# Performance work log

Hardware: AMD Instinct MI355X
Metric: run time of the kernel (lower is better)

Reference implementation:

```python
import jax, jax.numpy as jnp
import numpy as np

NEG = jnp.finfo(jnp.float32).min


def setup_inputs() -> dict:
    key = jax.random.key(0)
    k1, k2, k3 = jax.random.split(key, 3)
    B, H, S, D = 1, 12, 4096, 64
    query = jax.random.normal(k1, (B, H, S, D), dtype=jnp.float32)
    key_t = jax.random.normal(k2, (B, H, S, D), dtype=jnp.float32)
    value = jax.random.normal(k3, (B, H, S, D), dtype=jnp.float32)
    attention_mask = jnp.ones((B, S), dtype=jnp.int32)  # 2D mask -> causal branch
    return {
        "query": query,
        "key": key_t,
        "value": value,
        "attention_mask": attention_mask,
        "sliding_window": 128,
    }


def reference(query, key, value, attention_mask, sliding_window):
    # query/key/value: [B, H, S, D]
    B, H, S, D = query.shape
    scaling = 1.0 / jnp.sqrt(jnp.float32(D))
    # QK^T scaled: [B, H, S, S]
    attn_weights = jnp.einsum("bhqd,bhkd->bhqk", query, key) * scaling
    i = jnp.arange(S)[:, None]
    j = jnp.arange(S)[None, :]
    # 2D attention_mask branch: causal triu mask (values of mask not used)
    causal_mask = jnp.where(j > i, NEG, 0.0).astype(attn_weights.dtype)
    attn_weights = attn_weights + causal_mask
    # sliding window: row i allows columns [max(0, i - sw + 1), i]
    sw_allowed = (j >= i - sliding_window + 1) & (j <= i)
    sw_mask = jnp.where(sw_allowed, 0.0, NEG).astype(jnp.float32)
    attn_weights = attn_weights + sw_mask[None, None, :, :]
    # softmax in float32, cast back to query dtype
    attn_weights = jax.nn.softmax(attn_weights.astype(jnp.float32), axis=-1).astype(query.dtype)
    # probs @ V, then transpose heads: [B, S, H, D]
    attn_output = jnp.einsum("bhqk,bhkd->bhqd", attn_weights, value)
    attn_output = jnp.transpose(attn_output, (0, 2, 1, 3))
    return attn_output, attn_weights
```

## Files before the change

### kernel.cpp

```cpp
#include <hip/hip_runtime.h>
#include <math.h>

#define NH 12
#define SEQ 4096
#define DIM 64
#define SW 128
#define RPB 16
#define TPB 256
#define MAXK (RPB + SW - 1)
#define PSTRIDE 144
#define BAND_BLOCKS (NH * (SEQ / RPB))
#define FILL_BLOCKS 8448
#define PERIOD 15
#define NCHUNK ((size_t)NH * SEQ * (SEQ / 4))

typedef float v4f __attribute__((ext_vector_type(4)));

__global__ __launch_bounds__(TPB, 3)
void attn_fused3(const float* __restrict__ Q, const float* __restrict__ K,
                 const float* __restrict__ V, float* __restrict__ Wout,
                 float* __restrict__ Oout) {
    __shared__ v4f K4[MAXK * 16];
    __shared__ __align__(16) float Qs[RPB * DIM];
    __shared__ v4f Ps4[RPB * (PSTRIDE / 4)];
    float* Ps = (float*)Ps4;

    const int grp = blockIdx.x / PERIOD;
    const int rem = blockIdx.x % PERIOD;

    if (rem >= 4) {
        const size_t fid    = (size_t)grp * 11 + (rem - 4);
        const size_t tid0   = fid * TPB + threadIdx.x;
        const size_t stride = (size_t)FILL_BLOCKS * TPB;
        const float4 z = make_float4(0.f, 0.f, 0.f, 0.f);
        for (size_t idx = tid0; idx < NCHUNK; idx += stride) {
            const int ci = (int)(idx & 1023);
            const int i  = (int)((idx >> 10) & 4095);
            const int w0 = max(0, i - (SW - 1));
            if (ci < (w0 >> 2) || ci > (i >> 2)) {
                *(float4*)((float*)Wout + idx * 4) = z;
            }
        }
        return;
    }

    const int bid  = grp * 4 + rem;
    const int h    = bid / (SEQ / RPB);
    const int tile = bid % (SEQ / RPB);
    const int r0   = tile * RPB;
    const int kLo  = max(0, r0 - (SW - 1));
    const int nK   = r0 + RPB - kLo;

    const float* Qh = Q + (size_t)h * SEQ * DIM;
    const float* Kh = K + (size_t)h * SEQ * DIM;
    const float* Vh = V + (size_t)h * SEQ * DIM;
    const int tid = threadIdx.x;

    for (int idx = tid; idx < MAXK * 16; idx += TPB) {
        const int c = idx >> 4, b = idx & 15;
        const int src = min(c, nK - 1);
        K4[c * 16 + (b ^ (c & 15))] =
            *(const v4f*)(Kh + (size_t)(kLo + src) * DIM + b * 4);
    }
    {
        const int r = tid >> 4, b = tid & 15;
        *(v4f*)&Qs[r * 64 + b * 4] = *(const v4f*)(Qh + (size_t)(r0 + r) * DIM + b * 4);
    }
    __syncthreads();

    const int wave = tid >> 6;
    const int lane = tid & 63;
    const float scale = 0.125f;
    const int rbase = wave * 4;

    {
        const int base = rbase * (PSTRIDE / 4);
        for (int idx = lane; idx < 4 * (PSTRIDE / 4); idx += 64)
            Ps4[base + idx] = (v4f){0.f, 0.f, 0.f, 0.f};
    }

    for (int t = 0; t < 4; ++t) {
        const int r  = rbase + t;
        const int i  = r0 + r;
        const int w0 = max(0, i - (SW - 1));
        const int c0 = w0 - kLo;

        v4f q[16];
        #pragma unroll
        for (int b = 0; b < 16; ++b) q[b] = *(const v4f*)&Qs[r * 64 + b * 4];

        const int cA = c0 + lane;
        float accA = 0.f;
        #pragma unroll
        for (int b = 0; b < 16; ++b) {
            const v4f kv = K4[cA * 16 + (b ^ (cA & 15))];
            accA += q[b].x * kv.x + q[b].y * kv.y + q[b].z * kv.z + q[b].w * kv.w;
        }
        const int colA = w0 + lane;
        const float s0 = (colA <= i) ? accA * scale : -INFINITY;

        const int cB = cA + 64;
        float accB = 0.f;
        #pragma unroll
        for (int b = 0; b < 16; ++b) {
            const v4f kv = K4[cB * 16 + (b ^ (cB & 15))];
            accB += q[b].x * kv.x + q[b].y * kv.y + q[b].z * kv.z + q[b].w * kv.w;
        }
        const int colB = colA + 64;
        const float s1 = (colB <= i) ? accB * scale : -INFINITY;

        float m = fmaxf(s0, s1);
        #pragma unroll
        for (int o = 32; o > 0; o >>= 1) m = fmaxf(m, __shfl_xor(m, o, 64));
        const float e0 = __expf(s0 - m);
        const float e1 = __expf(s1 - m);
        float sum = e0 + e1;
        #pragma unroll
        for (int o = 32; o > 0; o >>= 1) sum += __shfl_xor(sum, o, 64);
        const float inv = 1.0f / sum;
        const float p0 = e0 * inv, p1 = e1 * inv;

        Ps[r * PSTRIDE + c0 + lane]      = p0;
        Ps[r * PSTRIDE + c0 + 64 + lane] = p1;

        float* wrow = Wout + ((size_t)h * SEQ + i) * SEQ;
        if (colA <= i) wrow[colA] = p0;
        if (colB <= i) wrow[colB] = p1;
        if (lane < 4) {
            const int cl = (w0 & ~3) + lane;
            if (cl < w0) wrow[cl] = 0.f;
            const int ch = i + 1 + lane;
            if (ch <= (i | 3)) wrow[ch] = 0.f;
        }
    }

    {
        const int i0  = r0 + rbase;
        const int u0k = max(0, i0 - (SW - 1)) - kLo;
        const int u1k = i0 + 3 - kLo;
        const int nch = (u1k - u0k + 4) >> 2;
        const int q4  = lane >> 4, l16 = lane & 15;

        v4f a0 = {0.f,0.f,0.f,0.f}, a1 = a0, a2 = a0, a3 = a0;
        for (int k = 0; k < nch; ++k) {
            const int cc   = u0k + k * 4 + q4;
            const int vrow = min(kLo + cc, SEQ - 1);
            const v4f vv = *(const v4f*)(Vh + (size_t)vrow * DIM + l16 * 4);
            a0 += Ps[(rbase + 0) * PSTRIDE + cc] * vv;
            a1 += Ps[(rbase + 1) * PSTRIDE + cc] * vv;
            a2 += Ps[(rbase + 2) * PSTRIDE + cc] * vv;
            a3 += Ps[(rbase + 3) * PSTRIDE + cc] * vv;
        }
        #pragma unroll
        for (int c = 0; c < 4; ++c) {
            float v;
            v = a0[c]; v += __shfl_xor(v, 16, 64); v += __shfl_xor(v, 32, 64); a0[c] = v;
            v = a1[c]; v += __shfl_xor(v, 16, 64); v += __shfl_xor(v, 32, 64); a1[c] = v;
            v = a2[c]; v += __shfl_xor(v, 16, 64); v += __shfl_xor(v, 32, 64); a2[c] = v;
            v = a3[c]; v += __shfl_xor(v, 16, 64); v += __shfl_xor(v, 32, 64); a3[c] = v;
        }
        const v4f o = (q4 == 0) ? a0 : (q4 == 1) ? a1 : (q4 == 2) ? a2 : a3;
        *(v4f*)(Oout + ((size_t)(i0 + q4) * NH + h) * DIM + l16 * 4) = o;
    }
}

extern "C" void kernel_launch(void* const* d_in, const int* in_sizes, int n_in,
                              void* d_out, int out_size, void* d_ws, size_t ws_size,
                              hipStream_t stream) {
    const float* Q = (const float*)d_in[0];
    const float* K = (const float*)d_in[1];
    const float* V = (const float*)d_in[2];

    float* Oout = (float*)d_out;
    float* Wout = (float*)d_out + (size_t)SEQ * NH * DIM;

    dim3 grid(BAND_BLOCKS + FILL_BLOCKS);
    attn_fused3<<<grid, TPB, 0, stream>>>(Q, K, V, Wout, Oout);
}
```

Before: 857.7 us.

## Split zero-fill into separate unconditional kernel before banded attention kernel

The single interleaved kernel that mixed band-attention blocks with masked zero-fill blocks is replaced by two launches. The first is a dedicated kernel that writes zeros over the entire attention-weight matrix using unrolled, unconditional float4 stores. The second is the band attention kernel, which then overwrites the band; stream ordering guarantees it runs after the fill. This removes the per-chunk index arithmetic, branches and partial-edge zero writes, in exchange for redundantly writing the band region twice and adding a second launch with no overlap between fill and compute.

New measurement: 899.0 us. +4.8%, slower.

```diff
diff --git a/kernel.cpp b/kernel.cpp
--- a/kernel.cpp
+++ b/kernel.cpp
@@ -10,41 +10,36 @@
 #define MAXK (RPB + SW - 1)
 #define PSTRIDE 144
 #define BAND_BLOCKS (NH * (SEQ / RPB))
-#define FILL_BLOCKS 8448
-#define PERIOD 15
+#define FILL_GRID 8192
 #define NCHUNK ((size_t)NH * SEQ * (SEQ / 4))
 
 typedef float v4f __attribute__((ext_vector_type(4)));
 
+__global__ __launch_bounds__(TPB)
+void fill_w(v4f* __restrict__ W) {
+    const v4f z = {0.f, 0.f, 0.f, 0.f};
+    size_t base = (size_t)blockIdx.x * 1024 + threadIdx.x;
+    const size_t sweep = (size_t)FILL_GRID * 1024;
+    #pragma unroll
+    for (int s = 0; s < 6; ++s) {
+        v4f* p = W + base + (size_t)s * sweep;
+        p[0]   = z;
+        p[256] = z;
+        p[512] = z;
+        p[768] = z;
+    }
+}
+
 __global__ __launch_bounds__(TPB, 3)
-void attn_fused3(const float* __restrict__ Q, const float* __restrict__ K,
-                 const float* __restrict__ V, float* __restrict__ Wout,
-                 float* __restrict__ Oout) {
+void attn_band(const float* __restrict__ Q, const float* __restrict__ K,
+               const float* __restrict__ V, float* __restrict__ Wout,
+               float* __restrict__ Oout) {
     __shared__ v4f K4[MAXK * 16];
     __shared__ __align__(16) float Qs[RPB * DIM];
     __shared__ v4f Ps4[RPB * (PSTRIDE / 4)];
     float* Ps = (float*)Ps4;
 
-    const int grp = blockIdx.x / PERIOD;
-    const int rem = blockIdx.x % PERIOD;
-
-    if (rem >= 4) {
-        const size_t fid    = (size_t)grp * 11 + (rem - 4);
-        const size_t tid0   = fid * TPB + threadIdx.x;
-        const size_t stride = (size_t)FILL_BLOCKS * TPB;
-        const float4 z = make_float4(0.f, 0.f, 0.f, 0.f);
-        for (size_t idx = tid0; idx < NCHUNK; idx += stride) {
-            const int ci = (int)(idx & 1023);
-            const int i  = (int)((idx >> 10) & 4095);
-            const int w0 = max(0, i - (SW - 1));
-            if (ci < (w0 >> 2) || ci > (i >> 2)) {
-                *(float4*)((float*)Wout + idx * 4) = z;
-            }
-        }
-        return;
-    }
-
-    const int bid  = grp * 4 + rem;
+    const int bid  = blockIdx.x;
     const int h    = bid / (SEQ / RPB);
     const int tile = bid % (SEQ / RPB);
     const int r0   = tile * RPB;
@@ -126,12 +121,6 @@
         float* wrow = Wout + ((size_t)h * SEQ + i) * SEQ;
         if (colA <= i) wrow[colA] = p0;
         if (colB <= i) wrow[colB] = p1;
-        if (lane < 4) {
-            const int cl = (w0 & ~3) + lane;
-            if (cl < w0) wrow[cl] = 0.f;
-            const int ch = i + 1 + lane;
-            if (ch <= (i | 3)) wrow[ch] = 0.f;
-        }
     }
 
     {
@@ -174,6 +163,6 @@
     float* Oout = (float*)d_out;
     float* Wout = (float*)d_out + (size_t)SEQ * NH * DIM;
 
-    dim3 grid(BAND_BLOCKS + FILL_BLOCKS);
-    attn_fused3<<<grid, TPB, 0, stream>>>(Q, K, V, Wout, Oout);
+    fill_w<<<FILL_GRID, TPB, 0, stream>>>((v4f*)Wout);
+    attn_band<<<BAND_BLOCKS, TPB, 0, stream>>>(Q, K, V, Wout, Oout);
 }
```
